# Kernel tuning notes

Measured on AMD Instinct MI355X. Metric: run time of the kernel, lower is better.

The kernel has to match this reference:

```python
import jax, jax.numpy as jnp
import numpy as np

VAR_N, LEVELS, NCELLS, PRED_N = 4, 17, 56, 12
D = VAR_N * LEVELS          # 68
FLAT = VAR_N * D            # 272 = ntiles * interm in CrossConnector
T = 4096
DT = 0.1                    # fused-ODE solver step of the LTC cell


def _var_encoder(x, w1, b1, w2, b2, w3, b3, w4, b4, w5, b5):
    # nn.Sequential(Linear, ReLU, Linear, ReLU, Linear, ReLU, Linear, ReLU, Linear)
    h = jax.nn.relu(x @ w1 + b1)
    h = jax.nn.relu(h @ w2 + b2)
    h = jax.nn.relu(h @ w3 + b3)
    h = jax.nn.relu(h @ w4 + b4)
    return h @ w5 + b5


def _run_ltc(seq, wx, wh, b, a, tau, wout, bout):
    def cell(h, u):
        f = jax.nn.sigmoid(u @ wx + h @ wh + b)           # gated synaptic activation
        return (h + DT * f * a) / (1.0 + DT * (1.0 / (tau + 0.5) + f))

    def step_obs(h, u):
        h2 = cell(h, u)
        return h2, h2 @ wout + bout

    hT, vs1 = jax.lax.scan(step_obs, jnp.zeros((NCELLS,), seq.dtype), seq)

    def step_pred(carry, _):
        h, v = carry
        h2 = cell(h, v)
        v2 = h2 @ wout + bout
        return (h2, v2), v2

    _, vs2 = jax.lax.scan(step_pred, (hT, vs1[-1]), None, length=PRED_N)
    return jnp.concatenate([vs1, vs2], axis=0)        # (T+PRED_N, LEVELS)


def setup_inputs() -> dict:
    key = jax.random.key(0)
    ks = iter(jax.random.split(key, 64))
    d = {"x": jax.random.normal(next(ks), (T, D), jnp.float32)}

    def add_ve(prefix, inp, out):
        dims = [(inp, inp), (inp, inp), (inp, out), (out, out), (out, out)]
        for i, (fi, fo) in enumerate(dims, 1):
            d[f"{prefix}w{i}"] = jax.random.normal(next(ks), (fi, fo), jnp.float32) / np.sqrt(fi)
            d[f"{prefix}b{i}"] = jax.random.normal(next(ks), (fo,), jnp.float32) * 0.01

    add_ve("p", D, D)          # preproc  VarEncoder(68,68)
    add_ve("c1", LEVELS, D)    # CrossConnector inner VarEncoder(17,68)
    add_ve("c2", FLAT, D)      # CrossConnector outer VarEncoder(272,68)

    d["ltc_wx"] = jax.random.normal(next(ks), (VAR_N, LEVELS, NCELLS), jnp.float32) / np.sqrt(LEVELS)
    d["ltc_wh"] = jax.random.normal(next(ks), (VAR_N, NCELLS, NCELLS), jnp.float32) / np.sqrt(NCELLS)
    d["ltc_b"] = jax.random.normal(next(ks), (VAR_N, NCELLS), jnp.float32) * 0.01
    d["ltc_a"] = jax.random.normal(next(ks), (VAR_N, NCELLS), jnp.float32)
    d["ltc_tau"] = jax.random.uniform(next(ks), (VAR_N, NCELLS), jnp.float32)
    d["ltc_wout"] = jax.random.normal(next(ks), (VAR_N, NCELLS, LEVELS), jnp.float32) / np.sqrt(NCELLS)
    d["ltc_bout"] = jax.random.normal(next(ks), (VAR_N, LEVELS), jnp.float32) * 0.01
    return d


def reference(x, pw1, pb1, pw2, pb2, pw3, pb3, pw4, pb4, pw5, pb5,
              c1w1, c1b1, c1w2, c1b2, c1w3, c1b3, c1w4, c1b4, c1w5, c1b5,
              c2w1, c2b1, c2w2, c2b2, c2w3, c2b3, c2w4, c2b4, c2w5, c2b5,
              ltc_wx, ltc_wh, ltc_b, ltc_a, ltc_tau, ltc_wout, ltc_bout):
    pre = _var_encoder(x, pw1, pb1, pw2, pb2, pw3, pb3, pw4, pb4, pw5, pb5)   # (T, 68)
    xs = pre.reshape(VAR_N, -1, LEVELS)                                       # (4, T, 17) row-major, as torch.reshape
    vs = jax.vmap(_run_ltc)(xs, ltc_wx, ltc_wh, ltc_b, ltc_a, ltc_tau,
                            ltc_wout, ltc_bout)                               # (4, T+12, 17)
    vs = jnp.transpose(vs, (1, 0, 2))                                         # (T+12, 4, 17)
    y = jax.nn.relu(_var_encoder(vs, c1w1, c1b1, c1w2, c1b2, c1w3, c1b3,
                                 c1w4, c1b4, c1w5, c1b5))                     # (T+12, 4, 68)
    y = y.reshape(y.shape[0], -1)                                             # (T+12, 272)
    return _var_encoder(y, c2w1, c2b1, c2w2, c2b2, c2w3, c2b3,
                        c2w4, c2b4, c2w5, c2b5)                               # (T+12, 68)
```

## Files before the change

### kernel.cpp

```cpp
#include <hip/hip_runtime.h>
#include <hip/hip_bf16.h>
#include <math.h>

#define VAR_N 4
#define LEVELS 17
#define NCELLS 56
#define PRED_N 12
#define TSTEPS 4096
#define DT 0.1f
#define RPB 8
#define LOG2E 1.44269504088896340736f

static __device__ __forceinline__ float rl(float x, int lane) {
    return __int_as_float(__builtin_amdgcn_readlane(__float_as_int(x), lane));
}
static __device__ __forceinline__ float rcpf(float x) {
    return __builtin_amdgcn_rcpf(x);
}

template <int S>
__global__ void mlp5_kernel(const float* __restrict__ in, float* __restrict__ out,
                            const float* __restrict__ w1, const float* __restrict__ b1,
                            const float* __restrict__ w2, const float* __restrict__ b2,
                            const float* __restrict__ w3, const float* __restrict__ b3,
                            const float* __restrict__ w4, const float* __restrict__ b4,
                            const float* __restrict__ w5, const float* __restrict__ b5,
                            int nrows, int d0, int d1, int d2, int d3, int d4, int d5,
                            int relu_last) {
    extern __shared__ float lds[];
    float* bufA = lds;
    float* bufB = lds + RPB * S;
    const int r0 = blockIdx.x * RPB;
    const int tid = threadIdx.x;
    const int bt = blockDim.x;

    for (int idx = tid; idx < RPB * d0; idx += bt) {
        int r = idx / d0, c = idx - r * d0;
        int gr = r0 + r;
        bufA[r * S + c] = (gr < nrows) ? in[(size_t)gr * d0 + c] : 0.f;
    }
    __syncthreads();

    const float* Ws[5] = {w1, w2, w3, w4, w5};
    const float* Bs[5] = {b1, b2, b3, b4, b5};
    int dins[5] = {d0, d1, d2, d3, d4};
    int douts[5] = {d1, d2, d3, d4, d5};

    for (int L = 0; L < 5; ++L) {
        const float* __restrict__ W = Ws[L];
        const float* __restrict__ B = Bs[L];
        const int din = dins[L], dout = douts[L];
        const bool act = (L < 4) || (relu_last != 0);
        for (int j = tid; j < dout; j += bt) {
            float acc[RPB];
            float bj = B[j];
#pragma unroll
            for (int r = 0; r < RPB; ++r) acc[r] = bj;
            for (int k = 0; k < din; ++k) {
                float wv = W[(size_t)k * dout + j];
#pragma unroll
                for (int r = 0; r < RPB; ++r)
                    acc[r] = fmaf(bufA[r * S + k], wv, acc[r]);
            }
#pragma unroll
            for (int r = 0; r < RPB; ++r) {
                float vo = acc[r];
                if (act) vo = fmaxf(vo, 0.f);
                bufB[r * S + j] = vo;
            }
        }
        __syncthreads();
        float* t = bufA; bufA = bufB; bufB = t;
    }

    for (int idx = tid; idx < RPB * d5; idx += bt) {
        int r = idx / d5, c = idx - r * d5;
        int gr = r0 + r;
        if (gr < nrows) out[(size_t)gr * d5 + c] = bufA[r * S + c];
    }
}

__global__ void gprep_kernel(const float* __restrict__ pre, const float* __restrict__ wx,
                             const float* __restrict__ b, float* __restrict__ g) {
    int idx = blockIdx.x * blockDim.x + threadIdx.x;
    if (idx >= VAR_N * NCELLS * TSTEPS) return;
    int t = idx % TSTEPS;
    int rem = idx / TSTEPS;
    int j = rem % NCELLS;
    int v = rem / NCELLS;
    const float* u = pre + (size_t)(v * 1024 + (t >> 2)) * 68 + (t & 3) * LEVELS;
    float acc = b[v * NCELLS + j];
#pragma unroll
    for (int l = 0; l < LEVELS; ++l)
        acc = fmaf(u[l], wx[(v * LEVELS + l) * NCELLS + j], acc);
    g[idx] = acc * LOG2E;
}

__global__ void __launch_bounds__(64, 1) scan_kernel(
    const float* __restrict__ g, const float* __restrict__ wh,
    const float* __restrict__ a, const float* __restrict__ tau,
    const float* __restrict__ wx, const float* __restrict__ wout,
    const float* __restrict__ bout, const float* __restrict__ b,
    float* __restrict__ H, float* __restrict__ vs_t) {
    typedef float v2 __attribute__((ext_vector_type(2)));
    const int v = blockIdx.x;
    const int lane = threadIdx.x;
    const bool active = lane < NCELLS;
    const int j = active ? lane : (NCELLS - 1);
    __shared__ __align__(16) float hbuf[64];

    v2 whp[28];
#pragma unroll
    for (int q = 0; q < 28; ++q) {
        float w0 = active ? wh[((size_t)v * NCELLS + 2 * q + 0) * NCELLS + lane] * LOG2E : 0.f;
        float w1 = active ? wh[((size_t)v * NCELLS + 2 * q + 1) * NCELLS + lane] * LOG2E : 0.f;
        v2 t; t.x = w0; t.y = w1;
        whp[q] = t;
    }
    const float alpha = active ? DT * a[v * NCELLS + lane] : 0.f;
    const float cden = active ? 1.f + DT / (tau[v * NCELLS + lane] + 0.5f) : 1.f;

    const float4* __restrict__ gv4 = (const float4*)(g + ((size_t)v * NCELLS + j) * TSTEPS);
    float* __restrict__ hp = H + (size_t)v * TSTEPS * NCELLS + lane;

    auto cell = [&](float h, float gcur) -> float {
        hbuf[lane] = h;
        const float4* h4 = (const float4*)hbuf;
        float4 hv[14];
#pragma unroll
        for (int q = 0; q < 14; ++q) hv[q] = h4[q];
        v2 a0 = {0.f, 0.f}, a1 = {0.f, 0.f}, a2 = {0.f, 0.f}, a3 = {0.f, 0.f};
#pragma unroll
        for (int q = 0; q < 7; ++q) {
            float4 hq0 = hv[2 * q];
            float4 hq1 = hv[2 * q + 1];
            v2 p0; p0.x = hq0.x; p0.y = hq0.y;
            v2 p1; p1.x = hq0.z; p1.y = hq0.w;
            v2 p2; p2.x = hq1.x; p2.y = hq1.y;
            v2 p3; p3.x = hq1.z; p3.y = hq1.w;
            a0 = __builtin_elementwise_fma(p0, whp[4 * q + 0], a0);
            a1 = __builtin_elementwise_fma(p1, whp[4 * q + 1], a1);
            a2 = __builtin_elementwise_fma(p2, whp[4 * q + 2], a2);
            a3 = __builtin_elementwise_fma(p3, whp[4 * q + 3], a3);
        }
        v2 s = (a0 + a1) + (a2 + a3);
        float z2 = gcur + s.x + s.y;
        float e = __builtin_amdgcn_exp2f(-z2);
        float f = rcpf(1.f + e);
        return fmaf(alpha, f, h) * rcpf(fmaf(DT, f, cden));
    };

    float h = 0.f;
    float4 gq = gv4[0];
    for (int tq = 0; tq < TSTEPS / 4; ++tq) {
        float4 gn = gq;
        if (tq + 1 < TSTEPS / 4) gn = gv4[tq + 1];
        h = cell(h, gq.x); if (active) hp[0 * NCELLS] = h;
        h = cell(h, gq.y); if (active) hp[1 * NCELLS] = h;
        h = cell(h, gq.z); if (active) hp[2 * NCELLS] = h;
        h = cell(h, gq.w); if (active) hp[3 * NCELLS] = h;
        hp += 4 * NCELLS;
        gq = gn;
    }

    float wxcol[LEVELS];
#pragma unroll
    for (int l = 0; l < LEVELS; ++l)
        wxcol[l] = active ? wx[(v * LEVELS + l) * NCELLS + lane] * LOG2E : 0.f;
    float wtc[NCELLS];
#pragma unroll
    for (int jj = 0; jj < NCELLS; ++jj)
        wtc[jj] = (lane < LEVELS) ? wout[((size_t)v * NCELLS + jj) * LEVELS + lane] : 0.f;
    const float bj = active ? b[v * NCELLS + lane] * LOG2E : 0.f;
    const float boutl = (lane < LEVELS) ? bout[v * LEVELS + lane] : 0.f;

    float vv = boutl;
#pragma unroll
    for (int jj = 0; jj < NCELLS; ++jj) vv = fmaf(rl(h, jj), wtc[jj], vv);

    for (int i = 0; i < PRED_N; ++i) {
        float z2 = bj;
#pragma unroll
        for (int l = 0; l < LEVELS; ++l) z2 = fmaf(rl(vv, l), wxcol[l], z2);
#pragma unroll
        for (int k = 0; k < NCELLS; ++k) {
            float wk = (k & 1) ? whp[k >> 1].y : whp[k >> 1].x;
            z2 = fmaf(rl(h, k), wk, z2);
        }
        float e = __builtin_amdgcn_exp2f(-z2);
        float f = rcpf(1.f + e);
        h = fmaf(alpha, f, h) * rcpf(fmaf(DT, f, cden));
        vv = boutl;
#pragma unroll
        for (int jj = 0; jj < NCELLS; ++jj) vv = fmaf(rl(h, jj), wtc[jj], vv);
        if (lane < LEVELS)
            vs_t[((size_t)(TSTEPS + i) * VAR_N + v) * LEVELS + lane] = vv;
    }
}

__global__ void proj_kernel(const float* __restrict__ H, const float* __restrict__ wout,
                            const float* __restrict__ bout, float* __restrict__ vs_t) {
    int idx = blockIdx.x * blockDim.x + threadIdx.x;
    if (idx >= VAR_N * TSTEPS * LEVELS) return;
    int l = idx % LEVELS;
    int rem = idx / LEVELS;
    int t = rem % TSTEPS;
    int v = rem / TSTEPS;
    const float* hrow = H + ((size_t)v * TSTEPS + t) * NCELLS;
    float acc = bout[v * LEVELS + l];
#pragma unroll
    for (int jj = 0; jj < NCELLS; ++jj)
        acc = fmaf(hrow[jj], wout[(v * NCELLS + jj) * LEVELS + l], acc);
    vs_t[((size_t)t * VAR_N + v) * LEVELS + l] = acc;
}

extern "C" void kernel_launch(void* const* d_in, const int* in_sizes, int n_in,
                              void* d_out, int out_size, void* d_ws, size_t ws_size,
                              hipStream_t stream) {
    const float* x = (const float*)d_in[0];
    const float* pw[5] = {(const float*)d_in[1], (const float*)d_in[3], (const float*)d_in[5],
                          (const float*)d_in[7], (const float*)d_in[9]};
    const float* pb[5] = {(const float*)d_in[2], (const float*)d_in[4], (const float*)d_in[6],
                          (const float*)d_in[8], (const float*)d_in[10]};
    const float* c1w[5] = {(const float*)d_in[11], (const float*)d_in[13], (const float*)d_in[15],
                           (const float*)d_in[17], (const float*)d_in[19]};
    const float* c1b[5] = {(const float*)d_in[12], (const float*)d_in[14], (const float*)d_in[16],
                           (const float*)d_in[18], (const float*)d_in[20]};
    const float* c2w[5] = {(const float*)d_in[21], (const float*)d_in[23], (const float*)d_in[25],
                           (const float*)d_in[27], (const float*)d_in[29]};
    const float* c2b[5] = {(const float*)d_in[22], (const float*)d_in[24], (const float*)d_in[26],
                           (const float*)d_in[28], (const float*)d_in[30]};
    const float* ltc_wx = (const float*)d_in[31];
    const float* ltc_wh = (const float*)d_in[32];
    const float* ltc_b = (const float*)d_in[33];
    const float* ltc_a = (const float*)d_in[34];
    const float* ltc_tau = (const float*)d_in[35];
    const float* ltc_wout = (const float*)d_in[36];
    const float* ltc_bout = (const float*)d_in[37];

    float* ws = (float*)d_ws;
    float* pre = ws;
    float* g = pre + 278528;
    float* H = g + 917504;
    float* vs_t = H + 917504;
    float* y1 = vs_t + 279344;
    float* out = (float*)d_out;

    const int TROWS = TSTEPS + PRED_N;

    {
        int nrows = TSTEPS;
        int blocks = (nrows + RPB - 1) / RPB;
        size_t shmem = 2 * RPB * 68 * sizeof(float);
        mlp5_kernel<68><<<blocks, 256, shmem, stream>>>(
            x, pre, pw[0], pb[0], pw[1], pb[1], pw[2], pb[2], pw[3], pb[3], pw[4], pb[4],
            nrows, 68, 68, 68, 68, 68, 68, 0);
    }
    {
        int n = VAR_N * NCELLS * TSTEPS;
        gprep_kernel<<<(n + 255) / 256, 256, 0, stream>>>(pre, ltc_wx, ltc_b, g);
    }
    scan_kernel<<<VAR_N, 64, 0, stream>>>(g, ltc_wh, ltc_a, ltc_tau, ltc_wx,
                                          ltc_wout, ltc_bout, ltc_b, H, vs_t);
    {
        int n = VAR_N * TSTEPS * LEVELS;
        proj_kernel<<<(n + 255) / 256, 256, 0, stream>>>(H, ltc_wout, ltc_bout, vs_t);
    }
    {
        int nrows = TROWS * VAR_N;
        int blocks = (nrows + RPB - 1) / RPB;
        size_t shmem = 2 * RPB * 68 * sizeof(float);
        mlp5_kernel<68><<<blocks, 256, shmem, stream>>>(
            vs_t, y1, c1w[0], c1b[0], c1w[1], c1b[1], c1w[2], c1b[2], c1w[3], c1b[3],
            c1w[4], c1b[4], nrows, 17, 17, 17, 68, 68, 68, 1);
    }
    {
        int nrows = TROWS;
        int blocks = (nrows + RPB - 1) / RPB;
        size_t shmem = 2 * RPB * 272 * sizeof(float);
        mlp5_kernel<272><<<blocks, 256, shmem, stream>>>(
            y1, out, c2w[0], c2b[0], c2w[1], c2b[1], c2w[2], c2b[2], c2w[3], c2b[3],
            c2w[4], c2b[4], nrows, 272, 272, 272, 68, 68, 68, 0);
    }
}
```

Before: 1.213 ms.

## Split recurrent dot between LDS and readlane, fold sigmoid reciprocal, unroll MLP k-loop

In the serial LTC scan, the hidden-state matvec is split: 40 of the 56 hidden values are still read back from LDS as float4 vectors, and the last 16 are broadcast with readlane against weights held in registers. This lets scalar-unit broadcasts overlap LDS latency on the critical path. The cell update is rewritten algebraically to multiply numerator and denominator by (1+e), which removes one reciprocal per step. The exponent is clamped at -80 to avoid overflow. The MLP kernel's inner k-loop is also unrolled by 4 with float4 LDS reads, which assumes 16-byte alignment of each row offset.

```diff
diff --git a/kernel.cpp b/kernel.cpp
--- a/kernel.cpp
+++ b/kernel.cpp
@@ -56,7 +56,22 @@
             float bj = B[j];
 #pragma unroll
             for (int r = 0; r < RPB; ++r) acc[r] = bj;
-            for (int k = 0; k < din; ++k) {
+            int k = 0;
+            for (; k + 4 <= din; k += 4) {
+                float w0v = W[(size_t)(k + 0) * dout + j];
+                float w1v = W[(size_t)(k + 1) * dout + j];
+                float w2v = W[(size_t)(k + 2) * dout + j];
+                float w3v = W[(size_t)(k + 3) * dout + j];
+#pragma unroll
+                for (int r = 0; r < RPB; ++r) {
+                    const float4 hx = *(const float4*)(bufA + r * S + k);
+                    acc[r] = fmaf(hx.x, w0v,
+                              fmaf(hx.y, w1v,
+                               fmaf(hx.z, w2v,
+                                fmaf(hx.w, w3v, acc[r]))));
+                }
+            }
+            for (; k < din; ++k) {
                 float wv = W[(size_t)k * dout + j];
 #pragma unroll
                 for (int r = 0; r < RPB; ++r)
@@ -109,14 +124,19 @@
     const int j = active ? lane : (NCELLS - 1);
     __shared__ __align__(16) float hbuf[64];
 
-    v2 whp[28];
-#pragma unroll
-    for (int q = 0; q < 28; ++q) {
+    v2 whp[20];
+#pragma unroll
+    for (int q = 0; q < 20; ++q) {
         float w0 = active ? wh[((size_t)v * NCELLS + 2 * q + 0) * NCELLS + lane] * LOG2E : 0.f;
         float w1 = active ? wh[((size_t)v * NCELLS + 2 * q + 1) * NCELLS + lane] * LOG2E : 0.f;
         v2 t; t.x = w0; t.y = w1;
         whp[q] = t;
     }
+    float whs[16];
+#pragma unroll
+    for (int q = 0; q < 16; ++q)
+        whs[q] = active ? wh[((size_t)v * NCELLS + 40 + q) * NCELLS + lane] * LOG2E : 0.f;
+
     const float alpha = active ? DT * a[v * NCELLS + lane] : 0.f;
     const float cden = active ? 1.f + DT / (tau[v * NCELLS + lane] + 0.5f) : 1.f;
 
@@ -125,13 +145,22 @@
 
     auto cell = [&](float h, float gcur) -> float {
         hbuf[lane] = h;
+        float rr0 = 0.f, rr1 = 0.f, rr2 = 0.f, rr3 = 0.f;
+#pragma unroll
+        for (int q = 0; q < 4; ++q) {
+            rr0 = fmaf(rl(h, 40 + 4 * q + 0), whs[4 * q + 0], rr0);
+            rr1 = fmaf(rl(h, 40 + 4 * q + 1), whs[4 * q + 1], rr1);
+            rr2 = fmaf(rl(h, 40 + 4 * q + 2), whs[4 * q + 2], rr2);
+            rr3 = fmaf(rl(h, 40 + 4 * q + 3), whs[4 * q + 3], rr3);
+        }
+        float zrl = (rr0 + rr1) + (rr2 + rr3);
         const float4* h4 = (const float4*)hbuf;
-        float4 hv[14];
-#pragma unroll
-        for (int q = 0; q < 14; ++q) hv[q] = h4[q];
+        float4 hv[10];
+#pragma unroll
+        for (int q = 0; q < 10; ++q) hv[q] = h4[q];
         v2 a0 = {0.f, 0.f}, a1 = {0.f, 0.f}, a2 = {0.f, 0.f}, a3 = {0.f, 0.f};
 #pragma unroll
-        for (int q = 0; q < 7; ++q) {
+        for (int q = 0; q < 5; ++q) {
             float4 hq0 = hv[2 * q];
             float4 hq1 = hv[2 * q + 1];
             v2 p0; p0.x = hq0.x; p0.y = hq0.y;
@@ -144,10 +173,13 @@
             a3 = __builtin_elementwise_fma(p3, whp[4 * q + 3], a3);
         }
         v2 s = (a0 + a1) + (a2 + a3);
-        float z2 = gcur + s.x + s.y;
-        float e = __builtin_amdgcn_exp2f(-z2);
-        float f = rcpf(1.f + e);
-        return fmaf(alpha, f, h) * rcpf(fmaf(DT, f, cden));
+        float z2 = ((gcur + zrl) + s.x) + s.y;
+        float zc = fmaxf(z2, -80.f);
+        float e = __builtin_amdgcn_exp2f(-zc);
+        float t1 = 1.f + e;
+        float num = fmaf(h, t1, alpha);
+        float den = fmaf(cden, t1, DT);
+        return num * rcpf(den);
     };
 
     float h = 0.f;
@@ -184,12 +216,13 @@
         for (int l = 0; l < LEVELS; ++l) z2 = fmaf(rl(vv, l), wxcol[l], z2);
 #pragma unroll
         for (int k = 0; k < NCELLS; ++k) {
-            float wk = (k & 1) ? whp[k >> 1].y : whp[k >> 1].x;
+            float wk = (k < 40) ? ((k & 1) ? whp[k >> 1].y : whp[k >> 1].x) : whs[k - 40];
             z2 = fmaf(rl(h, k), wk, z2);
         }
-        float e = __builtin_amdgcn_exp2f(-z2);
-        float f = rcpf(1.f + e);
-        h = fmaf(alpha, f, h) * rcpf(fmaf(DT, f, cden));
+        float zc = fmaxf(z2, -80.f);
+        float e = __builtin_amdgcn_exp2f(-zc);
+        float t1 = 1.f + e;
+        h = fmaf(h, t1, alpha) * rcpf(fmaf(cden, t1, DT));
         vv = boutl;
 #pragma unroll
         for (int jj = 0; jj < NCELLS; ++jj) vv = fmaf(rl(h, jj), wtc[jj], vv);
```

Result: slower. 1.249 ms (+2.9%).
